# Kernel optimization log

Measured on AMD Instinct MI355X. Metric: run time of the kernel, lower is better.

The kernel has to match this reference:

```python
import jax, jax.numpy as jnp
import numpy as np

B, N, C, DIN, DOUT = 16, 65536, 256, 16, 16  # ratio = N // C = 256 nodes per cluster


def setup_inputs() -> dict:
    key = jax.random.key(0)
    k1, k2, k3, k4, k5 = jax.random.split(key, 5)
    stdv = 1.0 / np.sqrt(DOUT)
    x = jax.random.normal(k1, (B, N, DIN), dtype=jnp.float32)
    # parameters, pre-reshaped: torch w_diag (in*out, C) with out-major io axis -> (out, in, C)
    w_diag = jax.random.uniform(k2, (DOUT, DIN, C), jnp.float32, -stdv, stdv)
    w_off = jax.random.uniform(k3, (DOUT, DIN, C, C), jnp.float32, -stdv, stdv)
    b1 = jax.random.uniform(k4, (DOUT,), jnp.float32, -stdv, stdv)
    # flatten_ids(cluster_ids): a permutation putting each cluster's nodes contiguous
    permute_ids = jax.random.permutation(k5, N)
    return {"x": x, "w_diag": w_diag, "w_off": w_off, "b1": b1, "permute_ids": permute_ids}


def reference(x, w_diag, w_off, b1, permute_ids):
    # Faithful to: W = rearrange(kron(diag_embed(w_diag), I_r)) + (1/N) rearrange(kron(w_off, 1_{rxr}))
    # out = inv_permute( reshape( W @ flatten(permute(x)) ) ) + b1,
    # computed via the block-constant structure instead of materializing the (Dout*N, Din*N) W.
    Bq, Nn, Din = x.shape
    Dout, _, Cc = w_diag.shape
    ratio = Nn // Cc
    inv_permute = jnp.argsort(permute_ids)
    xp = x[:, permute_ids, :]                       # (B, N, Din), cluster-contiguous
    xc = xp.reshape(Bq, Cc, ratio, Din)             # (B, C, r, Din)
    # diagonal blocks: per-cluster Din->Dout mixing, identity over within-cluster index
    out_diag = jnp.einsum('oic,bcri->bcro', w_diag, xc)   # (B, C, r, Dout)
    # off blocks: constant within each (cluster j, cluster k) block -> use cluster sums
    s = xc.sum(axis=2)                              # (B, C, Din)
    out_off = jnp.einsum('oick,bki->bco', w_off, s) / Nn  # (B, C, Dout)
    out = out_diag + out_off[:, :, None, :]         # broadcast over within-cluster index
    out = out.reshape(Bq, Nn, Dout)[:, inv_permute, :] + b1[None, None, :]
    return out
```

## Files before the change

kernel.cpp:

```cpp
#include <hip/hip_runtime.h>

#define B_    16
#define N_    65536
#define C_    256
#define DIN_  16
#define DOUT_ 16


__global__ __launch_bounds__(256) void k_sum_prep(
    const float* __restrict__ x, const float* __restrict__ w_diag,
    const int* __restrict__ P, float* __restrict__ s,
    float* __restrict__ wd_t, int* __restrict__ c_of_n)
{
    int bid = blockIdx.x;
    int t = threadIdx.x;
    if (bid >= B_ * C_) {
        int r = bid - B_ * C_;
        if (r < 256) {
            int o = r >> 4, i = r & 15;
            wd_t[t * 256 + i * 16 + o] = w_diag[r * C_ + t];
        } else {
            int k = r - 256;
            c_of_n[P[k * 256 + t]] = k;
        }
        return;
    }
    int b = bid >> 8;
    int k = bid & (C_ - 1);
    int q  = t & 3;
    int rg = t >> 2;
    float4 acc = make_float4(0.f, 0.f, 0.f, 0.f);
    const int jbase = k << 8;
    #pragma unroll
    for (int m = 0; m < 4; ++m) {
        int n = P[jbase + rg + 64 * m];
        const float4* row =
            reinterpret_cast<const float4*>(x + ((size_t)(b * N_ + n)) * DIN_);
        float4 v = row[q];
        acc.x += v.x; acc.y += v.y; acc.z += v.z; acc.w += v.w;
    }
    #pragma unroll
    for (int mask = 4; mask <= 32; mask <<= 1) {
        acc.x += __shfl_xor(acc.x, mask, 64);
        acc.y += __shfl_xor(acc.y, mask, 64);
        acc.z += __shfl_xor(acc.z, mask, 64);
        acc.w += __shfl_xor(acc.w, mask, 64);
    }
    __shared__ float4 part[4][4];
    int lane = t & 63, wave = t >> 6;
    if (lane < 4) part[wave][lane] = acc;
    __syncthreads();
    if (t < 16) {
        int qq = t >> 2, comp = t & 3;
        float v = 0.f;
        #pragma unroll
        for (int w = 0; w < 4; ++w) {
            const float* p = reinterpret_cast<const float*>(&part[w][qq]);
            v += p[comp];
        }
        int i = qq * 4 + comp;
        s[i * (B_ * C_) + b * C_ + k] = v;
    }
}

__global__ __launch_bounds__(256) void k_off(
    const float* __restrict__ w_off, const float* __restrict__ s,
    const float* __restrict__ b1, float* __restrict__ off)
{
    const int c  = blockIdx.x;
    const int t  = threadIdx.x;
    const int kq = t & 63;
    const int wq = t >> 6;

    __shared__ float4 slds[2][1024];

    const float4* s4 = reinterpret_cast<const float4*>(s);
    const float4* w4 = reinterpret_cast<const float4*>(w_off);

    int wbase[4];
    #pragma unroll
    for (int o4 = 0; o4 < 4; ++o4)
        wbase[o4] = (wq * 4 + o4) * 262144 + c * 64 + kq;

    float acc[64];
    #pragma unroll
    for (int z = 0; z < 64; ++z) acc[z] = 0.f;

    float4 sA[4], sB[4], wA[4], wB[4], s0[4];

    #pragma unroll
    for (int j = 0; j < 4; ++j) s0[j] = s4[t + 256 * j];
    #pragma unroll
    for (int o4 = 0; o4 < 4; ++o4) wA[o4] = w4[wbase[o4]];
    #pragma unroll
    for (int j = 0; j < 4; ++j) sA[j] = s4[1024 + t + 256 * j];
    #pragma unroll
    for (int j = 0; j < 4; ++j) slds[0][t + 256 * j] = s0[j];
    __syncthreads();

#define K2_BODY(I, WC, WN, SR, SI, RB, WBUF)                                   \
    {                                                                          \
        if ((I) + 2 < DIN_) {                                                  \
            _Pragma("unroll")                                                  \
            for (int j = 0; j < 4; ++j)                                        \
                SI[j] = s4[((I) + 2) * 1024 + t + 256 * j];                    \
        }                                                                      \
        if ((I) + 1 < DIN_) {                                                  \
            _Pragma("unroll")                                                  \
            for (int o4 = 0; o4 < 4; ++o4)                                     \
                WN[o4] = w4[wbase[o4] + ((I) + 1) * 16384];                    \
        }                                                                      \
        _Pragma("unroll")                                                      \
        for (int b = 0; b < 16; ++b) {                                         \
            float4 sv = slds[RB][b * 64 + kq];                                 \
            _Pragma("unroll")                                                  \
            for (int o4 = 0; o4 < 4; ++o4)                                     \
                acc[o4 * 16 + b] += WC[o4].x * sv.x + WC[o4].y * sv.y          \
                                  + WC[o4].z * sv.z + WC[o4].w * sv.w;         \
        }                                                                      \
        if ((I) + 1 < DIN_) {                                                  \
            _Pragma("unroll")                                                  \
            for (int j = 0; j < 4; ++j)                                        \
                slds[WBUF][t + 256 * j] = SR[j];                               \
            __syncthreads();                                                   \
        }                                                                      \
    }

    #pragma unroll 1
    for (int ih = 0; ih < DIN_ / 2; ++ih) {
        const int i0 = ih * 2;
        K2_BODY(i0,     wA, wB, sA, sB, 0, 1)
        K2_BODY(i0 + 1, wB, wA, sB, sA, 1, 0)
    }
#undef K2_BODY

#define FOLD(MASK, CNT)                                                        \
    {                                                                          \
        const bool hi_ = (kq & (MASK)) != 0;                                   \
        _Pragma("unroll")                                                      \
        for (int j = 0; j < (CNT); ++j) {                                      \
            float keep = hi_ ? acc[j + (CNT)] : acc[j];                        \
            float send = hi_ ? acc[j] : acc[j + (CNT)];                        \
            acc[j] = keep + __shfl_xor(send, (MASK), 64);                      \
        }                                                                      \
    }
    FOLD(1, 32) FOLD(2, 16) FOLD(4, 8) FOLD(8, 4) FOLD(16, 2) FOLD(32, 1)
#undef FOLD

    int j = ((kq >> 5) & 1) | ((kq >> 3) & 2) | ((kq >> 1) & 4)
          | ((kq << 1) & 8) | ((kq << 3) & 16) | ((kq << 5) & 32);
    int b  = j & 15;
    int o4 = j >> 4;
    int o  = wq * 4 + o4;
    off[((b << 8) + c) * DOUT_ + o] = acc[0] * (1.0f / (float)N_) + b1[o];
}

__global__ __launch_bounds__(256) void k_apply_seq(
    const float* __restrict__ x, const int* __restrict__ c_of_n,
    const float* __restrict__ wd_t, const float* __restrict__ off,
    float* __restrict__ out)
{
    int t = threadIdx.x;
    int lr = t >> 2, q = t & 3;
    int n = blockIdx.x * 64 + lr;
    int c = c_of_n[n];

    const float4* wd4 = reinterpret_cast<const float4*>(wd_t);
    float4 wds[16];
    #pragma unroll
    for (int i = 0; i < 16; ++i) wds[i] = wd4[c * 64 + i * 4 + q];

    const float4* x4   = reinterpret_cast<const float4*>(x);
    const float4* off4 = reinterpret_cast<const float4*>(off);
    float4* out4       = reinterpret_cast<float4*>(out);

    #pragma unroll 2
    for (int b = 0; b < B_; ++b) {
        size_t rowbase = ((size_t)(b * N_ + n)) * 4;
        float4 x0 = x4[rowbase + 0];
        float4 x1 = x4[rowbase + 1];
        float4 x2 = x4[rowbase + 2];
        float4 x3 = x4[rowbase + 3];
        float4 acc = off4[((size_t)((b << 8) + c)) * 4 + q];
        float xv[16];
        xv[0]=x0.x; xv[1]=x0.y; xv[2]=x0.z; xv[3]=x0.w;
        xv[4]=x1.x; xv[5]=x1.y; xv[6]=x1.z; xv[7]=x1.w;
        xv[8]=x2.x; xv[9]=x2.y; xv[10]=x2.z; xv[11]=x2.w;
        xv[12]=x3.x; xv[13]=x3.y; xv[14]=x3.z; xv[15]=x3.w;
        #pragma unroll
        for (int i = 0; i < 16; ++i) {
            acc.x += xv[i] * wds[i].x;
            acc.y += xv[i] * wds[i].y;
            acc.z += xv[i] * wds[i].z;
            acc.w += xv[i] * wds[i].w;
        }
        out4[rowbase + q] = acc;
    }
}

extern "C" void kernel_launch(void* const* d_in, const int* in_sizes, int n_in,
                              void* d_out, int out_size, void* d_ws, size_t ws_size,
                              hipStream_t stream) {
    const float* x      = (const float*)d_in[0];
    const float* w_diag = (const float*)d_in[1];
    const float* w_off  = (const float*)d_in[2];
    const float* b1     = (const float*)d_in[3];
    const int*   P      = (const int*)d_in[4];
    float* out    = (float*)d_out;
    float* s      = (float*)d_ws;
    float* off    = s + 65536;
    float* wd_t   = off + 65536;
    int*   c_of_n = (int*)(wd_t + 65536);

    k_sum_prep<<<B_ * C_ + 512, 256, 0, stream>>>(x, w_diag, P, s, wd_t, c_of_n);
    k_off<<<C_, 256, 0, stream>>>(w_off, s, b1, off);
    k_apply_seq<<<N_ / 64, 256, 0, stream>>>(x, c_of_n, wd_t, off, out);
}
```

Before: 224.6 us.

## Split k_off work across more blocks and waves with smaller per-thread accumulators

k_off now launches two blocks per cluster, each covering half of the output channels, and uses 512 threads per block. Each wave handles four batches and four outputs, so the per-thread accumulator shrinks from 64 to 16 registers and the shuffle fold tree gets shorter. The goal is more parallelism and occupancy for the w_off streaming, which previously ran on only 256 blocks on a GPU with many CUs. In exchange, each s slice is loaded into LDS twice as often, the block barrier spans more waves, and the loop is now fully unrolled.

```diff
diff --git a/kernel.cpp b/kernel.cpp
--- a/kernel.cpp
+++ b/kernel.cpp
@@ -63,14 +63,19 @@
     }
 }
 
-__global__ __launch_bounds__(256) void k_off(
+__global__ __launch_bounds__(512) void k_off(
     const float* __restrict__ w_off, const float* __restrict__ s,
     const float* __restrict__ b1, float* __restrict__ off)
 {
-    const int c  = blockIdx.x;
+    const int c  = (int)blockIdx.x >> 1;
+    const int og = (int)blockIdx.x & 1;
     const int t  = threadIdx.x;
     const int kq = t & 63;
-    const int wq = t >> 6;
+    const int w  = t >> 6;
+    const int oq = w & 1;
+    const int bh = w >> 1;
+    const int b0 = bh * 4;
+    const int o0 = og * 8 + oq * 4;
 
     __shared__ float4 slds[2][1024];
 
@@ -80,30 +85,31 @@
     int wbase[4];
     #pragma unroll
     for (int o4 = 0; o4 < 4; ++o4)
-        wbase[o4] = (wq * 4 + o4) * 262144 + c * 64 + kq;
-
-    float acc[64];
-    #pragma unroll
-    for (int z = 0; z < 64; ++z) acc[z] = 0.f;
-
-    float4 sA[4], sB[4], wA[4], wB[4], s0[4];
-
-    #pragma unroll
-    for (int j = 0; j < 4; ++j) s0[j] = s4[t + 256 * j];
-    #pragma unroll
-    for (int o4 = 0; o4 < 4; ++o4) wA[o4] = w4[wbase[o4]];
-    #pragma unroll
-    for (int j = 0; j < 4; ++j) sA[j] = s4[1024 + t + 256 * j];
-    #pragma unroll
-    for (int j = 0; j < 4; ++j) slds[0][t + 256 * j] = s0[j];
-    __syncthreads();
-
-#define K2_BODY(I, WC, WN, SR, SI, RB, WBUF)                                   \
+        wbase[o4] = (o0 + o4) * 262144 + c * 64 + kq;
+
+    float acc[16];
+    #pragma unroll
+    for (int z = 0; z < 16; ++z) acc[z] = 0.f;
+
+    float4 wA[4], wB[4], sA[2], sB[2];
+
+    {
+        float4 p0 = s4[t], p1 = s4[t + 512];
+        #pragma unroll
+        for (int o4 = 0; o4 < 4; ++o4) wA[o4] = w4[wbase[o4]];
+        sA[0] = s4[1024 + t];
+        sA[1] = s4[1024 + t + 512];
+        slds[0][t] = p0;
+        slds[0][t + 512] = p1;
+        asm volatile("s_waitcnt lgkmcnt(0)" ::: "memory");
+        __builtin_amdgcn_s_barrier();
+    }
+
+#define K2_BODY(I, WC, WN, SR, SI, RB)                                         \
     {                                                                          \
         if ((I) + 2 < DIN_) {                                                  \
-            _Pragma("unroll")                                                  \
-            for (int j = 0; j < 4; ++j)                                        \
-                SI[j] = s4[((I) + 2) * 1024 + t + 256 * j];                    \
+            SI[0] = s4[((I) + 2) * 1024 + t];                                  \
+            SI[1] = s4[((I) + 2) * 1024 + t + 512];                            \
         }                                                                      \
         if ((I) + 1 < DIN_) {                                                  \
             _Pragma("unroll")                                                  \
@@ -111,26 +117,25 @@
                 WN[o4] = w4[wbase[o4] + ((I) + 1) * 16384];                    \
         }                                                                      \
         _Pragma("unroll")                                                      \
-        for (int b = 0; b < 16; ++b) {                                         \
-            float4 sv = slds[RB][b * 64 + kq];                                 \
+        for (int bq = 0; bq < 4; ++bq) {                                       \
+            float4 sv = slds[RB][(b0 + bq) * 64 + kq];                         \
             _Pragma("unroll")                                                  \
             for (int o4 = 0; o4 < 4; ++o4)                                     \
-                acc[o4 * 16 + b] += WC[o4].x * sv.x + WC[o4].y * sv.y          \
+                acc[o4 * 4 + bq] += WC[o4].x * sv.x + WC[o4].y * sv.y          \
                                   + WC[o4].z * sv.z + WC[o4].w * sv.w;         \
         }                                                                      \
         if ((I) + 1 < DIN_) {                                                  \
-            _Pragma("unroll")                                                  \
-            for (int j = 0; j < 4; ++j)                                        \
-                slds[WBUF][t + 256 * j] = SR[j];                               \
-            __syncthreads();                                                   \
-        }                                                                      \
-    }
-
-    #pragma unroll 1
+            slds[(RB) ^ 1][t]       = SR[0];                                   \
+            slds[(RB) ^ 1][t + 512] = SR[1];                                   \
+            asm volatile("s_waitcnt lgkmcnt(0)" ::: "memory");                 \
+            __builtin_amdgcn_s_barrier();                                      \
+        }                                                                      \
+    }
+
+    #pragma unroll
     for (int ih = 0; ih < DIN_ / 2; ++ih) {
-        const int i0 = ih * 2;
-        K2_BODY(i0,     wA, wB, sA, sB, 0, 1)
-        K2_BODY(i0 + 1, wB, wA, sB, sA, 1, 0)
+        K2_BODY(2 * ih,     wA, wB, sA, sB, 0)
+        K2_BODY(2 * ih + 1, wB, wA, sB, sA, 1)
     }
 #undef K2_BODY
 
@@ -144,15 +149,17 @@
             acc[j] = keep + __shfl_xor(send, (MASK), 64);                      \
         }                                                                      \
     }
-    FOLD(1, 32) FOLD(2, 16) FOLD(4, 8) FOLD(8, 4) FOLD(16, 2) FOLD(32, 1)
+    FOLD(1, 8) FOLD(2, 4) FOLD(4, 2) FOLD(8, 1)
 #undef FOLD
-
-    int j = ((kq >> 5) & 1) | ((kq >> 3) & 2) | ((kq >> 1) & 4)
-          | ((kq << 1) & 8) | ((kq << 3) & 16) | ((kq << 5) & 32);
-    int b  = j & 15;
-    int o4 = j >> 4;
-    int o  = wq * 4 + o4;
-    off[((b << 8) + c) * DOUT_ + o] = acc[0] * (1.0f / (float)N_) + b1[o];
+    acc[0] += __shfl_xor(acc[0], 16, 64);
+    acc[0] += __shfl_xor(acc[0], 32, 64);
+
+    if (kq < 16) {
+        int j  = ((kq & 1) << 3) | ((kq & 2) << 1) | ((kq & 4) >> 1) | ((kq & 8) >> 3);
+        int b  = b0 + (j & 3);
+        int o  = o0 + (j >> 2);
+        off[((b << 8) + c) * DOUT_ + o] = acc[0] * (1.0f / (float)N_) + b1[o];
+    }
 }
 
 __global__ __launch_bounds__(256) void k_apply_seq(
@@ -213,6 +220,6 @@
     int*   c_of_n = (int*)(wd_t + 65536);
 
     k_sum_prep<<<B_ * C_ + 512, 256, 0, stream>>>(x, w_diag, P, s, wd_t, c_of_n);
-    k_off<<<C_, 256, 0, stream>>>(w_off, s, b1, off);
+    k_off<<<C_ * 2, 512, 0, stream>>>(w_off, s, b1, off);
     k_apply_seq<<<N_ / 64, 256, 0, stream>>>(x, c_of_n, wd_t, off, out);
 }
```

Result: faster. 208.3 us (-7.3%).
